# Performance work log

Measured on AMD Instinct MI355X. Metric: run time of the kernel, lower is better.

## Reference

```python
import jax, jax.numpy as jnp
import numpy as np

QMAX = 127.0


def setup_inputs() -> dict:
    key = jax.random.key(0)
    k1, k2, k3, k4, k5, k6 = jax.random.split(key, 6)
    B, IN, OUT = 8192, 4096, 4096
    # Quantized activation (uint8-range values stored as float, per-sample asymmetric quant)
    x_q = jax.random.randint(k1, (B, IN), 0, 256).astype(jnp.float32)
    x_scale = jax.random.uniform(k2, (B,), dtype=jnp.float32, minval=0.001, maxval=0.02)
    x_zp = jax.random.randint(k3, (B,), 0, 256).astype(jnp.float32)
    # Symmetric per-tensor int8 weight (values in [-127, 127]) + scalar scale
    w_q = jax.random.randint(k4, (OUT, IN), -127, 128).astype(jnp.float32)
    w_scale = jax.random.uniform(k5, (1,), dtype=jnp.float32, minval=0.001, maxval=0.02)
    fp_bias = jax.random.normal(k6, (OUT,), dtype=jnp.float32)
    return {"x_q": x_q, "x_scale": x_scale, "x_zp": x_zp, "w_q": w_q,
            "w_scale": w_scale, "fp_bias": fp_bias}


def reference(x_q, x_scale, x_zp, w_q, w_scale, fp_bias):
    # zero-point subtraction (per-sample)
    xt = x_q - x_zp[:, None]                      # [B, IN]
    # integer GEMM (values are integers held in float32)
    lin = xt @ w_q.T                              # [B, OUT]
    # integer bias: round(fp_bias / (w_scale * x_scale))
    qbias = jnp.round(fp_bias[None, :] / (w_scale[0] * x_scale[:, None]))  # [B, OUT]
    lin = lin + qbias
    # requantize: symmetric per-tensor int8
    s = jnp.max(jnp.abs(lin)) / QMAX
    q = jnp.clip(jnp.round(lin / s), -QMAX, QMAX)  # [B, OUT]
    out_scale = s * x_scale * w_scale[0]           # [B]
    zero_point = jnp.zeros_like(out_scale)
    return q, out_scale, zero_point
```

## Files before the change

### kernel.cpp

```cpp
#include <hip/hip_runtime.h>
#include <hip/hip_bf16.h>


typedef int i32x4 __attribute__((ext_vector_type(4)));

#define AS1 __attribute__((address_space(1)))
#define AS3 __attribute__((address_space(3)))

__device__ __forceinline__ void async16(const void* g, void* lds) {
    __builtin_amdgcn_global_load_lds((const AS1 void*)g, (AS3 void*)lds, 16, 0, 0);
}

__global__ void conv_x_kernel(const float4* __restrict__ xq, int* __restrict__ x8,
                              int* gmax, int n4) {
    int i = blockIdx.x * 256 + threadIdx.x;
    if (i == 0) *gmax = 0;
    if (i >= n4) return;
    float4 v = xq[i];
    int b0 = ((int)v.x - 128) & 255;
    int b1 = ((int)v.y - 128) & 255;
    int b2 = ((int)v.z - 128) & 255;
    int b3 = ((int)v.w - 128) & 255;
    x8[i] = b0 | (b1 << 8) | (b2 << 16) | (b3 << 24);
}

__global__ void conv_w_kernel(const float* __restrict__ wq, int* __restrict__ w8,
                              int* __restrict__ rowsum, int K) {
    int row = blockIdx.x;
    int t = threadIdx.x;
    const float4* src = (const float4*)(wq + (size_t)row * K);
    int* dst = w8 + (size_t)row * (K >> 2);
    int sum = 0;
    int passes = K >> 10;
    for (int p = 0; p < passes; ++p) {
        float4 v = src[p * 256 + t];
        int b0 = (int)v.x, b1 = (int)v.y, b2 = (int)v.z, b3 = (int)v.w;
        sum += b0 + b1 + b2 + b3;
        dst[p * 256 + t] = (b0 & 255) | ((b1 & 255) << 8) | ((b2 & 255) << 16) | ((b3 & 255) << 24);
    }
    #pragma unroll
    for (int m = 32; m; m >>= 1) sum += __shfl_xor(sum, m, 64);
    __shared__ int wsum[4];
    if ((t & 63) == 0) wsum[t >> 6] = sum;
    __syncthreads();
    if (t == 0) rowsum[row] = wsum[0] + wsum[1] + wsum[2] + wsum[3];
}

__global__ __launch_bounds__(256, 3) void gemm_i8_kernel(
    const char* __restrict__ x8, const char* __restrict__ w8,
    const int* __restrict__ w_rowsum,
    const float* __restrict__ x_scale, const float* __restrict__ x_zp,
    const float* __restrict__ fp_bias, const float* __restrict__ w_scale_p,
    int* __restrict__ lin_out, int* gmax, int N, int K) {
    __shared__ char ldsA[128 * 64];
    __shared__ char ldsB[128 * 64];
    __shared__ int s_bmax;

    const int t = threadIdx.x;
    const int w = t >> 6, l = t & 63;
    const int tm = blockIdx.y, tn = blockIdx.x;
    if (t == 0) s_bmax = 0;

    const int srow = t >> 2;
    const int slot = t & 3;
    const int kg = slot ^ ((srow >> 1) & 3);
    const char* gA = x8 + ((size_t)(tm * 128 + srow)) * K + kg * 16;
    const char* gB = w8 + ((size_t)(tn * 128 + srow)) * K + kg * 16;
    char* dstA0 = ldsA + w * 1024;
    char* dstA1 = ldsA + 4096 + w * 1024;
    char* dstB0 = ldsB + w * 1024;
    char* dstB1 = ldsB + 4096 + w * 1024;

    const int lane_lo = l & 15, lane_hi = l >> 4;
    const int wm = w >> 1, wn = w & 1;
    const int ar = wm * 64 + lane_lo;
    const int aoff = ar * 64 + (lane_hi ^ ((ar >> 1) & 3)) * 16;
    const int br = wn * 64 + lane_lo;
    const int boff = br * 64 + (lane_hi ^ ((br >> 1) & 3)) * 16;

    i32x4 acc[4][4] = {};

    const int KITERS = K >> 6;
    for (int kt = 0; kt < KITERS; ++kt) {
        const char* pa = gA + (size_t)kt * 64;
        const char* pb = gB + (size_t)kt * 64;
        async16(pa, dstA0);
        async16(pa + (size_t)64 * K, dstA1);
        async16(pb, dstB0);
        async16(pb + (size_t)64 * K, dstB1);
        __syncthreads();
        i32x4 af[4], bf[4];
        #pragma unroll
        for (int m = 0; m < 4; ++m) af[m] = *(const i32x4*)(ldsA + aoff + m * 1024);
        #pragma unroll
        for (int n = 0; n < 4; ++n) bf[n] = *(const i32x4*)(ldsB + boff + n * 1024);
        #pragma unroll
        for (int m = 0; m < 4; ++m)
            #pragma unroll
            for (int n = 0; n < 4; ++n)
                acc[m][n] = __builtin_amdgcn_mfma_i32_16x16x64_i8(af[m], bf[n], acc[m][n], 0, 0, 0);
        __syncthreads();
    }

    const float ws = *w_scale_p;
    const int rowg0 = tm * 128 + wm * 64 + lane_hi * 4;
    const int colg0 = tn * 128 + wn * 64 + lane_lo;
    float xs[16];
    int zz[16];
    #pragma unroll
    for (int m = 0; m < 4; ++m)
        #pragma unroll
        for (int j = 0; j < 4; ++j) {
            int r = rowg0 + m * 16 + j;
            xs[m * 4 + j] = x_scale[r];
            zz[m * 4 + j] = 128 - (int)x_zp[r];
        }
    int lmax = 0;
    #pragma unroll
    for (int n = 0; n < 4; ++n) {
        int col = colg0 + n * 16;
        float fb = fp_bias[col];
        int wrs = w_rowsum[col];
        #pragma unroll
        for (int m = 0; m < 4; ++m)
            #pragma unroll
            for (int j = 0; j < 4; ++j) {
                int idx = m * 4 + j;
                int qb = (int)rintf(fb / (ws * xs[idx]));
                int lin = acc[m][n][j] + zz[idx] * wrs + qb;
                int a = lin < 0 ? -lin : lin;
                lmax = a > lmax ? a : lmax;
                lin_out[(size_t)(rowg0 + m * 16 + j) * N + col] = lin;
            }
    }
    atomicMax(&s_bmax, lmax);
    __syncthreads();
    if (t == 0) atomicMax(gmax, s_bmax);
}

__global__ void requant_kernel(float4* qout, const int4* lin, const int* gmax, int n4) {
    int i = blockIdx.x * 256 + threadIdx.x;
    if (i >= n4) return;
    float s = (float)(*gmax) / 127.0f;
    int4 v = lin[i];
    float4 o;
    o.x = fminf(127.0f, fmaxf(-127.0f, rintf((float)v.x / s)));
    o.y = fminf(127.0f, fmaxf(-127.0f, rintf((float)v.y / s)));
    o.z = fminf(127.0f, fmaxf(-127.0f, rintf((float)v.z / s)));
    o.w = fminf(127.0f, fmaxf(-127.0f, rintf((float)v.w / s)));
    qout[i] = o;
}

__global__ void scale_kernel(float* __restrict__ out_scale, float* __restrict__ out_zp,
                             const float* __restrict__ x_scale,
                             const float* __restrict__ w_scale_p,
                             const int* gmax, int B) {
    int i = blockIdx.x * 256 + threadIdx.x;
    if (i >= B) return;
    float s = (float)(*gmax) / 127.0f;
    out_scale[i] = s * x_scale[i] * w_scale_p[0];
    out_zp[i] = 0.0f;
}

extern "C" void kernel_launch(void* const* d_in, const int* in_sizes, int n_in,
                              void* d_out, int out_size, void* d_ws, size_t ws_size,
                              hipStream_t stream) {
    const float* x_q     = (const float*)d_in[0];
    const float* x_scale = (const float*)d_in[1];
    const float* x_zp    = (const float*)d_in[2];
    const float* w_q     = (const float*)d_in[3];
    const float* w_scale = (const float*)d_in[4];
    const float* fp_bias = (const float*)d_in[5];

    const int B   = in_sizes[1];
    const int IN  = in_sizes[0] / B;
    const int OUT = in_sizes[5];

    float* q         = (float*)d_out;
    float* out_scale = q + (size_t)B * OUT;
    float* out_zp    = out_scale + B;

    char* ws    = (char*)d_ws;
    int* gmax   = (int*)ws;
    char* x8    = ws + 64;
    char* w8    = x8 + (size_t)B * IN;
    int* rowsum = (int*)(w8 + (size_t)OUT * IN);
    size_t needed = 64 + (size_t)B * IN + (size_t)OUT * IN + (size_t)OUT * 4;
    if (ws_size < needed) return;

    int n4x = (B * IN) >> 2;
    conv_x_kernel<<<(n4x + 255) / 256, 256, 0, stream>>>((const float4*)x_q, (int*)x8, gmax, n4x);
    conv_w_kernel<<<OUT, 256, 0, stream>>>(w_q, (int*)w8, rowsum, IN);

    dim3 grid(OUT / 128, B / 128);
    gemm_i8_kernel<<<grid, 256, 0, stream>>>(x8, w8, rowsum, x_scale, x_zp, fp_bias,
                                             w_scale, (int*)q, gmax, OUT, IN);

    int n4q = (B * OUT) >> 2;
    requant_kernel<<<(n4q + 255) / 256, 256, 0, stream>>>((float4*)q, (const int4*)q, gmax, n4q);
    scale_kernel<<<(B + 255) / 256, 256, 0, stream>>>(out_scale, out_zp, x_scale, w_scale, gmax, B);
}
```

Baseline: 266.5 us.

## Enlarge int8 GEMM tile to 256x256 with 4-stage async LDS pipeline

Reworks the int8 MFMA GEMM to use 256x256 output tiles with 512 threads, where each wave computes 128x64 (8x4 MFMA fragments). It adds a four-buffer LDS ring that prefetches three K-slices ahead, using explicit vmcnt waits and a single barrier per iteration, and raises wave priority around the MFMA block. A 1D grid with an XCD-aware block swizzle is also added. The aim is to hide global-load latency, cut barrier count and per-FLOP LDS traffic, and improve L2 reuse across chiplets. In exchange it uses 128KB of LDS per block and needs more accumulator registers, which limits occupancy.

After: 273.8 us. 2.8% more time.

```diff
diff --git a/kernel.cpp b/kernel.cpp
--- a/kernel.cpp
+++ b/kernel.cpp
@@ -46,92 +46,113 @@
     if (t == 0) rowsum[row] = wsum[0] + wsum[1] + wsum[2] + wsum[3];
 }
 
-__global__ __launch_bounds__(256, 3) void gemm_i8_kernel(
+__global__ __launch_bounds__(512, 2) void gemm_i8_kernel(
     const char* __restrict__ x8, const char* __restrict__ w8,
     const int* __restrict__ w_rowsum,
     const float* __restrict__ x_scale, const float* __restrict__ x_zp,
     const float* __restrict__ fp_bias, const float* __restrict__ w_scale_p,
     int* __restrict__ lin_out, int* gmax, int N, int K) {
-    __shared__ char ldsA[128 * 64];
-    __shared__ char ldsB[128 * 64];
+    __shared__ __align__(16) char lds[4][32768];
     __shared__ int s_bmax;
 
     const int t = threadIdx.x;
     const int w = t >> 6, l = t & 63;
-    const int tm = blockIdx.y, tn = blockIdx.x;
     if (t == 0) s_bmax = 0;
 
-    const int srow = t >> 2;
-    const int slot = t & 3;
-    const int kg = slot ^ ((srow >> 1) & 3);
-    const char* gA = x8 + ((size_t)(tm * 128 + srow)) * K + kg * 16;
-    const char* gB = w8 + ((size_t)(tn * 128 + srow)) * K + kg * 16;
-    char* dstA0 = ldsA + w * 1024;
-    char* dstA1 = ldsA + 4096 + w * 1024;
-    char* dstB0 = ldsB + w * 1024;
-    char* dstB1 = ldsB + 4096 + w * 1024;
+    const int nwg = gridDim.x;
+    const int bid = blockIdx.x;
+    int swz = bid;
+    if ((nwg & 7) == 0) { const int cpx = nwg >> 3; swz = (bid & 7) * cpx + (bid >> 3); }
+    const int ntn = N >> 8;
+    const int tm = swz / ntn, tn = swz % ntn;
+
+    const int nt = K >> 6;
+
+    const int srow = (w << 5) + (l >> 2);
+    const int phys = (l & 3) ^ ((l >> 3) & 3);
+    const char* pA0 = x8 + (size_t)(tm * 256 + srow) * K + phys * 16;
+    const char* pA1 = pA0 + (size_t)16 * K;
+    const char* pB0 = w8 + (size_t)(tn * 256 + srow) * K + phys * 16;
+    const char* pB1 = pB0 + (size_t)16 * K;
+    const int dA0 = (w << 11) + (l << 4);
+    const int dA1 = dA0 + 1024;
 
     const int lane_lo = l & 15, lane_hi = l >> 4;
-    const int wm = w >> 1, wn = w & 1;
-    const int ar = wm * 64 + lane_lo;
-    const int aoff = ar * 64 + (lane_hi ^ ((ar >> 1) & 3)) * 16;
-    const int br = wn * 64 + lane_lo;
-    const int boff = br * 64 + (lane_hi ^ ((br >> 1) & 3)) * 16;
-
-    i32x4 acc[4][4] = {};
-
-    const int KITERS = K >> 6;
-    for (int kt = 0; kt < KITERS; ++kt) {
-        const char* pa = gA + (size_t)kt * 64;
-        const char* pb = gB + (size_t)kt * 64;
-        async16(pa, dstA0);
-        async16(pa + (size_t)64 * K, dstA1);
-        async16(pb, dstB0);
-        async16(pb + (size_t)64 * K, dstB1);
-        __syncthreads();
-        i32x4 af[4], bf[4];
-        #pragma unroll
-        for (int m = 0; m < 4; ++m) af[m] = *(const i32x4*)(ldsA + aoff + m * 1024);
-        #pragma unroll
-        for (int n = 0; n < 4; ++n) bf[n] = *(const i32x4*)(ldsB + boff + n * 1024);
-        #pragma unroll
-        for (int m = 0; m < 4; ++m)
+    const int wm = w >> 2, wn = w & 3;
+    const int sl = (lane_hi ^ ((lane_lo >> 1) & 3)) << 4;
+    const int abase = (wm * 128 + lane_lo) * 64 + sl;
+    const int bbase = 16384 + (wn * 64 + lane_lo) * 64 + sl;
+
+    i32x4 acc[8][4] = {};
+
+    #pragma unroll
+    for (int g = 0; g < 3; ++g) {
+        char* buf = lds[g];
+        const size_t koff = (size_t)g * 64;
+        async16(pA0 + koff, buf + dA0);
+        async16(pA1 + koff, buf + dA1);
+        async16(pB0 + koff, buf + 16384 + dA0);
+        async16(pB1 + koff, buf + 16384 + dA1);
+    }
+
+    for (int j = 0; j < nt; ++j) {
+        asm volatile("s_waitcnt lgkmcnt(0)" ::: "memory");
+        if (j + 2 < nt)       asm volatile("s_waitcnt vmcnt(8)" ::: "memory");
+        else if (j + 2 == nt) asm volatile("s_waitcnt vmcnt(4)" ::: "memory");
+        else                  asm volatile("s_waitcnt vmcnt(0)" ::: "memory");
+        __builtin_amdgcn_s_barrier();
+        asm volatile("" ::: "memory");
+        if (j + 3 < nt) {
+            char* buf = lds[(j + 3) & 3];
+            const size_t koff = (size_t)(j + 3) * 64;
+            async16(pA0 + koff, buf + dA0);
+            async16(pA1 + koff, buf + dA1);
+            async16(pB0 + koff, buf + 16384 + dA0);
+            async16(pB1 + koff, buf + 16384 + dA1);
+        }
+        const char* buf = lds[j & 3];
+        i32x4 af[8], bf[4];
+        #pragma unroll
+        for (int m = 0; m < 8; ++m) af[m] = *(const i32x4*)(buf + abase + m * 1024);
+        #pragma unroll
+        for (int n = 0; n < 4; ++n) bf[n] = *(const i32x4*)(buf + bbase + n * 1024);
+        __builtin_amdgcn_s_setprio(1);
+        #pragma unroll
+        for (int m = 0; m < 8; ++m)
             #pragma unroll
             for (int n = 0; n < 4; ++n)
                 acc[m][n] = __builtin_amdgcn_mfma_i32_16x16x64_i8(af[m], bf[n], acc[m][n], 0, 0, 0);
-        __syncthreads();
+        __builtin_amdgcn_s_setprio(0);
     }
 
     const float ws = *w_scale_p;
-    const int rowg0 = tm * 128 + wm * 64 + lane_hi * 4;
-    const int colg0 = tn * 128 + wn * 64 + lane_lo;
-    float xs[16];
-    int zz[16];
-    #pragma unroll
-    for (int m = 0; m < 4; ++m)
-        #pragma unroll
-        for (int j = 0; j < 4; ++j) {
-            int r = rowg0 + m * 16 + j;
-            xs[m * 4 + j] = x_scale[r];
-            zz[m * 4 + j] = 128 - (int)x_zp[r];
+    const int rowg0 = tm * 256 + wm * 128 + lane_hi * 4;
+    const int colg0 = tn * 256 + wn * 64 + lane_lo;
+    float fb[4]; int wrs[4];
+    #pragma unroll
+    for (int n = 0; n < 4; ++n) {
+        fb[n] = fp_bias[colg0 + n * 16];
+        wrs[n] = w_rowsum[colg0 + n * 16];
+    }
+    int lmax = 0;
+    #pragma unroll
+    for (int m = 0; m < 8; ++m) {
+        #pragma unroll
+        for (int r = 0; r < 4; ++r) {
+            const int row = rowg0 + m * 16 + r;
+            const float xs = x_scale[row];
+            const int zz = 128 - (int)x_zp[row];
+            const float d = ws * xs;
+            int* orow = lin_out + (size_t)row * N + colg0;
+            #pragma unroll
+            for (int n = 0; n < 4; ++n) {
+                const int qb = (int)rintf(fb[n] / d);
+                const int lin = acc[m][n][r] + zz * wrs[n] + qb;
+                const int a = lin < 0 ? -lin : lin;
+                lmax = a > lmax ? a : lmax;
+                orow[n * 16] = lin;
+            }
         }
-    int lmax = 0;
-    #pragma unroll
-    for (int n = 0; n < 4; ++n) {
-        int col = colg0 + n * 16;
-        float fb = fp_bias[col];
-        int wrs = w_rowsum[col];
-        #pragma unroll
-        for (int m = 0; m < 4; ++m)
-            #pragma unroll
-            for (int j = 0; j < 4; ++j) {
-                int idx = m * 4 + j;
-                int qb = (int)rintf(fb / (ws * xs[idx]));
-                int lin = acc[m][n][j] + zz[idx] * wrs + qb;
-                int a = lin < 0 ? -lin : lin;
-                lmax = a > lmax ? a : lmax;
-                lin_out[(size_t)(rowg0 + m * 16 + j) * N + col] = lin;
-            }
     }
     atomicMax(&s_bmax, lmax);
     __syncthreads();
@@ -192,9 +213,9 @@
     conv_x_kernel<<<(n4x + 255) / 256, 256, 0, stream>>>((const float4*)x_q, (int*)x8, gmax, n4x);
     conv_w_kernel<<<OUT, 256, 0, stream>>>(w_q, (int*)w8, rowsum, IN);
 
-    dim3 grid(OUT / 128, B / 128);
-    gemm_i8_kernel<<<grid, 256, 0, stream>>>(x8, w8, rowsum, x_scale, x_zp, fp_bias,
-                                             w_scale, (int*)q, gmax, OUT, IN);
+    int nblocks = (B / 256) * (OUT / 256);
+    gemm_i8_kernel<<<nblocks, 512, 0, stream>>>(x8, w8, rowsum, x_scale, x_zp, fp_bias,
+                                                w_scale, (int*)q, gmax, OUT, IN);
 
     int n4q = (B * OUT) >> 2;
     requant_kernel<<<(n4q + 255) / 256, 256, 0, stream>>>((float4*)q, (const int4*)q, gmax, n4q);
```
